# Kernel tuning notes

Hardware: AMD Instinct MI355X
Metric: run time of the kernel (lower is better)

## Reference

```python
import jax, jax.numpy as jnp
import numpy as np

NEG_SLOPE = 0.2  # PyG GATConv default negative_slope


def _gat_layer(x, src, dst, n_nodes, W, a_src, a_dst, b):
    # x: [N, din]; src/dst: [E] (self-loops already included)
    h = x @ W                                  # [N, dout]
    s_src = h @ a_src                          # [N]
    s_dst = h @ a_dst                          # [N]
    e = jax.nn.leaky_relu(s_src[src] + s_dst[dst], NEG_SLOPE)  # [E]
    # per-target-node softmax over incoming edges (stable via segment max)
    m = jax.ops.segment_max(e, dst, num_segments=n_nodes)      # [N]
    a = jnp.exp(e - m[dst])                    # [E]
    denom = jax.ops.segment_sum(a, dst, num_segments=n_nodes)  # [N]
    msg = h[src] * a[:, None]                  # [E, dout]
    agg = jax.ops.segment_sum(msg, dst, num_segments=n_nodes)  # [N, dout]
    return agg / denom[:, None] + b


def setup_inputs() -> dict:
    key = jax.random.key(0)
    ks = jax.random.split(key, 16)
    N, E = 100000, 1600000
    in_dim, hid_dim, out_dim = 128, 128, 64
    x = jax.random.normal(ks[0], (N, in_dim), dtype=jnp.float32)
    edge_idx = jax.random.randint(ks[1], (2, E), 0, N, dtype=jnp.int32)

    def lin(k, din, dout):
        return jax.random.normal(k, (din, dout), dtype=jnp.float32) * (1.0 / np.sqrt(din))

    def att(k, dout):
        return jax.random.normal(k, (dout,), dtype=jnp.float32) * (1.0 / np.sqrt(dout))

    return {
        "x": x, "edge_idx": edge_idx,
        "W1": lin(ks[2], in_dim, hid_dim), "as1": att(ks[3], hid_dim), "ad1": att(ks[4], hid_dim), "b1": jnp.zeros((hid_dim,), jnp.float32),
        "W2": lin(ks[5], hid_dim, hid_dim), "as2": att(ks[6], hid_dim), "ad2": att(ks[7], hid_dim), "b2": jnp.zeros((hid_dim,), jnp.float32),
        "W3": lin(ks[8], hid_dim, out_dim), "as3": att(ks[9], out_dim), "ad3": att(ks[10], out_dim), "b3": jnp.zeros((out_dim,), jnp.float32),
    }


def reference(x, edge_idx, W1, as1, ad1, b1, W2, as2, ad2, b2, W3, as3, ad3, b3):
    N = x.shape[0]
    # add self-loops (PyG GATConv default add_self_loops=True)
    loops = jnp.arange(N, dtype=edge_idx.dtype)
    src = jnp.concatenate([edge_idx[0], loops])
    dst = jnp.concatenate([edge_idx[1], loops])
    h = _gat_layer(x, src, dst, N, W1, as1, ad1, b1)
    h = _gat_layer(h, src, dst, N, W2, as2, ad2, b2)
    h = _gat_layer(h, src, dst, N, W3, as3, ad3, b3)
    return jnp.mean(h, axis=-2)  # [out_dim]
```

## Files before the change

kernel.cpp:

```cpp
#include <hip/hip_runtime.h>

static inline int ceil_div(long long a, long long b) { return (int)((a + b - 1) / b); }

typedef __attribute__((ext_vector_type(8))) short bf16x8;
typedef __attribute__((ext_vector_type(4))) float f32x4;

#define TILE 8192
#define BKSH 9

__device__ __forceinline__ float lrelu(float t) { return t > 0.f ? t : 0.2f * t; }

__device__ __forceinline__ void atomAddF(float* p, float v) {
  unsafeAtomicAdd(p, v);
}

__device__ __forceinline__ unsigned int f2bf(float f) {
  unsigned int u = __float_as_uint(f);
  unsigned int r = ((u >> 16) & 1u) + 0x7fffu;
  return (u + r) >> 16;
}

__global__ void cvt_bf16(const float* __restrict__ X, unsigned short* __restrict__ Xb, int n4) {
  int i = blockIdx.x * blockDim.x + threadIdx.x;
  if (i < n4) {
    const float4 v = ((const float4*)X)[i];
    uint2 o;
    o.x = f2bf(v.x) | (f2bf(v.y) << 16);
    o.y = f2bf(v.z) | (f2bf(v.w) << 16);
    ((uint2*)Xb)[i] = o;
  }
}

__global__ void transpose_w(const float* __restrict__ W, unsigned short* __restrict__ Wt,
                            int DINv, int DOUTv) {
  int idx = blockIdx.x * blockDim.x + threadIdx.x;
  if (idx < DINv * DOUTv) {
    int k = idx / DOUTv, n = idx % DOUTv;
    Wt[n * DINv + k] = (unsigned short)f2bf(W[idx]);
  }
}

template<int DOUT>
__launch_bounds__(256)
__global__ void gemm_mfma(const unsigned short* __restrict__ Xb, const unsigned short* __restrict__ Wt,
                          const float* __restrict__ avs, const float* __restrict__ avd,
                          unsigned short* __restrict__ Hb, float* __restrict__ Ss,
                          float* __restrict__ Sd, int N, int RG) {
  constexpr int DIN = 128;
  constexpr int CG = DOUT / 64;
  const int wave = (int)((blockIdx.x * (unsigned)blockDim.x + threadIdx.x) >> 6);
  const int rg = wave / CG;
  const int cg = wave % CG;
  if (rg >= RG) return;
  const int lane = threadIdx.x & 63;
  const int l16 = lane & 15, quad = lane >> 4;
  const int row0 = rg * 64, colw0 = cg * 64;

  int xoff[4], woff[4];
#pragma unroll
  for (int t = 0; t < 4; t++) {
    int m = row0 + t * 16 + l16; if (m > N - 1) m = N - 1;
    xoff[t] = m * DIN + quad * 8;
    woff[t] = (colw0 + t * 16 + l16) * DIN + quad * 8;
  }

  f32x4 acc[4][4];
#pragma unroll
  for (int a = 0; a < 4; a++)
#pragma unroll
    for (int c = 0; c < 4; c++) acc[a][c] = (f32x4)0.f;

#pragma unroll
  for (int kk = 0; kk < 4; kk++) {
    bf16x8 aw[4], bx[4];
#pragma unroll
    for (int t = 0; t < 4; t++) aw[t] = *(const bf16x8*)(Wt + woff[t] + kk * 32);
#pragma unroll
    for (int t = 0; t < 4; t++) bx[t] = *(const bf16x8*)(Xb + xoff[t] + kk * 32);
#pragma unroll
    for (int wt = 0; wt < 4; wt++)
#pragma unroll
      for (int xt = 0; xt < 4; xt++)
        acc[wt][xt] = __builtin_amdgcn_mfma_f32_16x16x32_bf16(aw[wt], bx[xt], acc[wt][xt], 0, 0, 0);
  }

  float4 af[4], df[4];
#pragma unroll
  for (int wt = 0; wt < 4; wt++) {
    af[wt] = *(const float4*)(avs + colw0 + wt * 16 + quad * 4);
    df[wt] = *(const float4*)(avd + colw0 + wt * 16 + quad * 4);
  }
#pragma unroll
  for (int xt = 0; xt < 4; xt++) {
    const int m = row0 + xt * 16 + l16;
    float ps = 0.f, pd = 0.f;
#pragma unroll
    for (int wt = 0; wt < 4; wt++) {
      const f32x4 c = acc[wt][xt];
      ps += c[0]*af[wt].x + c[1]*af[wt].y + c[2]*af[wt].z + c[3]*af[wt].w;
      pd += c[0]*df[wt].x + c[1]*df[wt].y + c[2]*df[wt].z + c[3]*df[wt].w;
    }
    ps += __shfl_xor(ps, 16); ps += __shfl_xor(ps, 32);
    pd += __shfl_xor(pd, 16); pd += __shfl_xor(pd, 32);
    if (quad == 0 && m < N) { atomAddF(&Ss[m], ps); atomAddF(&Sd[m], pd); }
    if (m < N) {
      unsigned short* hp = Hb + (size_t)m * DOUT + colw0 + quad * 4;
#pragma unroll
      for (int wt = 0; wt < 4; wt++) {
        const f32x4 c = acc[wt][xt];
        uint2 o;
        o.x = f2bf(c[0]) | (f2bf(c[1]) << 16);
        o.y = f2bf(c[2]) | (f2bf(c[3]) << 16);
        *(uint2*)(hp + wt * 16) = o;
      }
    }
  }
}

__launch_bounds__(256)
__global__ void bucket_hist(const int* __restrict__ dstv, int* __restrict__ bh,
                            int E, int NBUK) {
  __shared__ int h[256];
  h[threadIdx.x] = 0;
  __syncthreads();
  const int base = blockIdx.x * TILE;
  const int end = min(E, base + TILE);
  for (int i = base + threadIdx.x; i < end; i += 256)
    atomicAdd(&h[dstv[i] >> BKSH], 1);
  __syncthreads();
  if (threadIdx.x < NBUK) bh[blockIdx.x * NBUK + threadIdx.x] = h[threadIdx.x];
}

__launch_bounds__(256)
__global__ void col_scan(int* __restrict__ bh, int* __restrict__ tot, int NBA, int NBUK) {
  __shared__ int sc[256];
  const int t = threadIdx.x;
  const int b = blockIdx.x;
  int carry = 0;
  for (int c0 = 0; c0 < NBA; c0 += 256) {
    const int idx = c0 + t;
    const int v = (idx < NBA) ? bh[idx * NBUK + b] : 0;
    sc[t] = v;
    __syncthreads();
    for (int off = 1; off < 256; off <<= 1) {
      int u = (t >= off) ? sc[t - off] : 0;
      __syncthreads();
      sc[t] += u;
      __syncthreads();
    }
    if (idx < NBA) bh[idx * NBUK + b] = carry + sc[t] - v;
    carry += sc[255];
    __syncthreads();
  }
  if (t == 0) tot[b] = carry;
}

__launch_bounds__(256)
__global__ void base_scan(const int* __restrict__ tot, int* __restrict__ bucketBase,
                          int* __restrict__ rowptr_N, int NBUK, int E) {
  __shared__ int sc[256];
  const int t = threadIdx.x;
  int carry = 0;
  for (int c0 = 0; c0 < NBUK; c0 += 256) {
    const int idx = c0 + t;
    const int v = (idx < NBUK) ? tot[idx] : 0;
    sc[t] = v;
    __syncthreads();
    for (int off = 1; off < 256; off <<= 1) {
      int u = (t >= off) ? sc[t - off] : 0;
      __syncthreads();
      sc[t] += u;
      __syncthreads();
    }
    if (idx < NBUK) bucketBase[idx] = carry + sc[t] - v;
    carry += sc[255];
    __syncthreads();
  }
  if (t == 0) { bucketBase[NBUK] = E; *rowptr_N = E; }
}

__launch_bounds__(256)
__global__ void bucket_scatter(const int* __restrict__ src, const int* __restrict__ dstv,
                               const int* __restrict__ bh, const int* __restrict__ bucketBase,
                               unsigned int* __restrict__ pairs, int E, int NBUK) {
  __shared__ int ofs[256];
  if (threadIdx.x < NBUK)
    ofs[threadIdx.x] = bh[blockIdx.x * NBUK + threadIdx.x] + bucketBase[threadIdx.x];
  __syncthreads();
  const int base = blockIdx.x * TILE;
  const int end = min(E, base + TILE);
  for (int i = base + threadIdx.x; i < end; i += 256) {
    const int d = dstv[i];
    const int pos = atomicAdd(&ofs[d >> BKSH], 1);
    pairs[pos] = ((unsigned int)src[i] << BKSH) | (unsigned int)(d & ((1 << BKSH) - 1));
  }
}

__launch_bounds__(256)
__global__ void region_build(const unsigned int* __restrict__ pairs,
                             const int* __restrict__ bucketBase,
                             int* __restrict__ rowptr, int* __restrict__ srcs, int N) {
  __shared__ int cnt[512], ofs[512], ps[256];
  const int t = threadIdx.x;
  const int r = blockIdx.x;
  const int p0 = bucketBase[r], p1 = bucketBase[r + 1];
  cnt[t] = 0; cnt[t + 256] = 0;
  __syncthreads();
  for (int i = p0 + t; i < p1; i += 256)
    atomicAdd(&cnt[pairs[i] & 511u], 1);
  __syncthreads();
  const int c0 = cnt[2 * t], c1 = cnt[2 * t + 1];
  const int pr = c0 + c1;
  ps[t] = pr;
  __syncthreads();
  for (int off = 1; off < 256; off <<= 1) {
    int v = (t >= off) ? ps[t - off] : 0;
    __syncthreads();
    ps[t] += v;
    __syncthreads();
  }
  const int pbase = ps[t] - pr;
  ofs[2 * t] = pbase; ofs[2 * t + 1] = pbase + c0;
  __syncthreads();
  {
    const int d0 = (r << BKSH) + t;
    if (d0 < N) rowptr[d0] = p0 + ofs[t];
    const int d1 = (r << BKSH) + t + 256;
    if (d1 < N) rowptr[d1] = p0 + ofs[t + 256];
  }
  __syncthreads();
  for (int i = p0 + t; i < p1; i += 256) {
    const unsigned int w = pairs[i];
    const int pos = atomicAdd(&ofs[w & 511u], 1);
    srcs[p0 + pos] = (int)(w >> BKSH);
  }
}

template<int DOUT, bool OBF>
__launch_bounds__(256)
__global__ void node_gather(const int* __restrict__ rowptr, const int* __restrict__ srcs,
                            const float* __restrict__ Ss, const float* __restrict__ Sd,
                            const unsigned short* __restrict__ Hb, const float* __restrict__ b,
                            float* __restrict__ out, unsigned short* __restrict__ outb, int N) {
  constexpr int EPL = DOUT / 16;
  constexpr int CAP = 64;
  __shared__ uint2 swL[16][CAP];

  const int l16 = threadIdx.x & 15;
  const int grp = threadIdx.x >> 4;
  const int node = blockIdx.x * 16 + grp;
  if (node >= N) return;

  const int r0 = rowptr[node], r1 = rowptr[node + 1];
  const int deg = r1 - r0;
  const int degc = min(deg, CAP);
  const float sd = Sd[node];
  const float eself = lrelu(Ss[node] + sd);

  float m = eself;
  for (int j0 = 0; j0 < deg; j0 += 16) {
    const int idx = j0 + l16;
    float e = -1e30f;
    if (idx < deg) {
      const int s = srcs[r0 + idx];
      e = lrelu(Ss[s] + sd);
      if (idx < CAP) swL[grp][idx] = make_uint2((unsigned)s, __float_as_uint(e));
    }
    m = fmaxf(m, e);
  }
#pragma unroll
  for (int off = 8; off; off >>= 1) m = fmaxf(m, __shfl_xor(m, off));

  const float wself = __expf(eself - m);
  float lsum = 0.f;
  for (int j0 = 0; j0 < degc; j0 += 16) {
    const int idx = j0 + l16;
    if (idx < degc) {
      uint2 sw = swL[grp][idx];
      const float w = __expf(__uint_as_float(sw.y) - m);
      sw.y = __float_as_uint(w);
      swL[grp][idx] = sw;
      lsum += w;
    }
  }
  for (int j0 = CAP; j0 < deg; j0 += 16) {
    const int idx = j0 + l16;
    if (idx < deg) {
      const int s = srcs[r0 + idx];
      lsum += __expf(lrelu(Ss[s] + sd) - m);
    }
  }
#pragma unroll
  for (int off = 8; off; off >>= 1) lsum += __shfl_xor(lsum, off);
  const float inv = 1.f / (lsum + wself);
  __syncthreads();

  float acc[EPL];
#pragma unroll
  for (int k = 0; k < EPL; k++) acc[k] = 0.f;

  const size_t colb = (size_t)l16 * EPL;
  int j = 0;
  for (; j + 4 <= degc; j += 4) {
    uint2 sw0 = swL[grp][j], sw1 = swL[grp][j+1], sw2 = swL[grp][j+2], sw3 = swL[grp][j+3];
    const unsigned short* p0 = Hb + (size_t)sw0.x * DOUT + colb;
    const unsigned short* p1 = Hb + (size_t)sw1.x * DOUT + colb;
    const unsigned short* p2 = Hb + (size_t)sw2.x * DOUT + colb;
    const unsigned short* p3 = Hb + (size_t)sw3.x * DOUT + colb;
    if (EPL == 8) {
      const uint4 u0 = *(const uint4*)p0, u1 = *(const uint4*)p1;
      const uint4 u2 = *(const uint4*)p2, u3 = *(const uint4*)p3;
      const float w0 = __uint_as_float(sw0.y), w1 = __uint_as_float(sw1.y);
      const float w2 = __uint_as_float(sw2.y), w3 = __uint_as_float(sw3.y);
      const unsigned int a0[4] = {u0.x,u0.y,u0.z,u0.w}, a1[4] = {u1.x,u1.y,u1.z,u1.w};
      const unsigned int a2[4] = {u2.x,u2.y,u2.z,u2.w}, a3[4] = {u3.x,u3.y,u3.z,u3.w};
#pragma unroll
      for (int k = 0; k < 4; k++) {
        acc[2*k]   += __uint_as_float(a0[k] << 16) * w0 + __uint_as_float(a1[k] << 16) * w1
                    + __uint_as_float(a2[k] << 16) * w2 + __uint_as_float(a3[k] << 16) * w3;
        acc[2*k+1] += __uint_as_float(a0[k] & 0xffff0000u) * w0 + __uint_as_float(a1[k] & 0xffff0000u) * w1
                    + __uint_as_float(a2[k] & 0xffff0000u) * w2 + __uint_as_float(a3[k] & 0xffff0000u) * w3;
      }
    } else {
      const uint2 u0 = *(const uint2*)p0, u1 = *(const uint2*)p1;
      const uint2 u2 = *(const uint2*)p2, u3 = *(const uint2*)p3;
      const float w0 = __uint_as_float(sw0.y), w1 = __uint_as_float(sw1.y);
      const float w2 = __uint_as_float(sw2.y), w3 = __uint_as_float(sw3.y);
      const unsigned int a0[2] = {u0.x,u0.y}, a1[2] = {u1.x,u1.y};
      const unsigned int a2[2] = {u2.x,u2.y}, a3[2] = {u3.x,u3.y};
#pragma unroll
      for (int k = 0; k < 2; k++) {
        acc[2*k]   += __uint_as_float(a0[k] << 16) * w0 + __uint_as_float(a1[k] << 16) * w1
                    + __uint_as_float(a2[k] << 16) * w2 + __uint_as_float(a3[k] << 16) * w3;
        acc[2*k+1] += __uint_as_float(a0[k] & 0xffff0000u) * w0 + __uint_as_float(a1[k] & 0xffff0000u) * w1
                    + __uint_as_float(a2[k] & 0xffff0000u) * w2 + __uint_as_float(a3[k] & 0xffff0000u) * w3;
      }
    }
  }
  for (; j < degc; j++) {
    const uint2 sw = swL[grp][j];
    const float w = __uint_as_float(sw.y);
    const unsigned short* pp = Hb + (size_t)sw.x * DOUT + colb;
#pragma unroll
    for (int k = 0; k < EPL / 2; k++) {
      const unsigned int u = ((const unsigned int*)pp)[k];
      acc[2*k]   += __uint_as_float(u << 16) * w;
      acc[2*k+1] += __uint_as_float(u & 0xffff0000u) * w;
    }
  }
  for (j = CAP; j < deg; j++) {
    const int s = srcs[r0 + j];
    const float w = __expf(lrelu(Ss[s] + sd) - m);
    const unsigned short* pp = Hb + (size_t)s * DOUT + colb;
#pragma unroll
    for (int k = 0; k < EPL / 2; k++) {
      const unsigned int u = ((const unsigned int*)pp)[k];
      acc[2*k]   += __uint_as_float(u << 16) * w;
      acc[2*k+1] += __uint_as_float(u & 0xffff0000u) * w;
    }
  }
  {
    const unsigned short* pp = Hb + (size_t)node * DOUT + colb;
#pragma unroll
    for (int k = 0; k < EPL / 2; k++) {
      const unsigned int u = ((const unsigned int*)pp)[k];
      acc[2*k]   += __uint_as_float(u << 16) * wself;
      acc[2*k+1] += __uint_as_float(u & 0xffff0000u) * wself;
    }
  }

  float o[EPL];
#pragma unroll
  for (int k = 0; k < EPL; k++) o[k] = acc[k] * inv + b[colb + k];
  if (OBF) {
    if (EPL == 8) {
      uint4 u;
      u.x = f2bf(o[0]) | (f2bf(o[1]) << 16);
      u.y = f2bf(o[2]) | (f2bf(o[3]) << 16);
      u.z = f2bf(o[4]) | (f2bf(o[5]) << 16);
      u.w = f2bf(o[6]) | (f2bf(o[7]) << 16);
      *(uint4*)(outb + (size_t)node * DOUT + colb) = u;
    } else {
      uint2 u;
      u.x = f2bf(o[0]) | (f2bf(o[1]) << 16);
      u.y = f2bf(o[2]) | (f2bf(o[3]) << 16);
      *(uint2*)(outb + (size_t)node * DOUT + colb) = u;
    }
  } else {
    float* op = out + (size_t)node * DOUT + colb;
#pragma unroll
    for (int k = 0; k < EPL; k += 4)
      *(float4*)(op + k) = make_float4(o[k], o[k+1], o[k+2], o[k+3]);
  }
}

__global__ void mean64(const float* __restrict__ Hf, float* __restrict__ out, int N, float scale) {
  __shared__ float sm[256];
  const int col = threadIdx.x & 63;
  const int seg = threadIdx.x >> 6;
  const int stride = gridDim.x * 4;
  float s = 0.f;
  for (int n = blockIdx.x * 4 + seg; n < N; n += stride) s += Hf[(size_t)n * 64 + col];
  sm[threadIdx.x] = s;
  __syncthreads();
  if (seg == 0) {
    float tot = sm[col] + sm[64 + col] + sm[128 + col] + sm[192 + col];
    atomAddF(&out[col], tot * scale);
  }
}

extern "C" void kernel_launch(void* const* d_in, const int* in_sizes, int n_in,
                              void* d_out, int out_size, void* d_ws, size_t ws_size,
                              hipStream_t stream) {
  const float* x   = (const float*)d_in[0];
  const int*   ei  = (const int*)d_in[1];
  const float* W1  = (const float*)d_in[2];
  const float* as1 = (const float*)d_in[3];
  const float* ad1 = (const float*)d_in[4];
  const float* b1  = (const float*)d_in[5];
  const float* W2  = (const float*)d_in[6];
  const float* as2 = (const float*)d_in[7];
  const float* ad2 = (const float*)d_in[8];
  const float* b2  = (const float*)d_in[9];
  const float* W3  = (const float*)d_in[10];
  const float* as3 = (const float*)d_in[11];
  const float* ad3 = (const float*)d_in[12];
  const float* b3  = (const float*)d_in[13];

  const int N = in_sizes[0] / 128;
  const int E = in_sizes[1] / 2;
  const int* src  = ei;
  const int* dstv = ei + E;
  const int RG = ceil_div(N, 64);
  const int NBA = ceil_div(E, TILE);
  const int NBUK = ceil_div(N, 1 << BKSH);

  float* p = (float*)d_ws;
  float* bufA = p; p += (size_t)N * 64;
  float* SsSd = p; p += (size_t)2 * N;
  float* Ss = SsSd, *Sd = SsSd + N;
  unsigned short* Xb = (unsigned short*)p; p += (size_t)N * 64;
  unsigned short* Hb = (unsigned short*)p; p += (size_t)N * 64;
  unsigned short* Wt1 = (unsigned short*)p; p += 128 * 128 / 2;
  unsigned short* Wt2 = (unsigned short*)p; p += 128 * 128 / 2;
  unsigned short* Wt3 = (unsigned short*)p; p += 128 * 64 / 2;
  int* ip = (int*)p;
  int* rowptr     = ip; ip += N + 1;
  int* bh         = ip; ip += (size_t)NBA * NBUK;
  int* tot        = ip; ip += NBUK;
  int* bucketBase = ip; ip += NBUK + 1;
  unsigned int* pairs = (unsigned int*)ip; ip += E;
  int* srcs       = ip; ip += E;

  bucket_hist<<<NBA, 256, 0, stream>>>(dstv, bh, E, NBUK);
  col_scan<<<NBUK, 256, 0, stream>>>(bh, tot, NBA, NBUK);
  base_scan<<<1, 256, 0, stream>>>(tot, bucketBase, rowptr + N, NBUK, E);
  bucket_scatter<<<NBA, 256, 0, stream>>>(src, dstv, bh, bucketBase, pairs, E, NBUK);
  region_build<<<NBUK, 256, 0, stream>>>(pairs, bucketBase, rowptr, srcs, N);

  transpose_w<<<ceil_div(128 * 128, 256), 256, 0, stream>>>(W1, Wt1, 128, 128);
  transpose_w<<<ceil_div(128 * 128, 256), 256, 0, stream>>>(W2, Wt2, 128, 128);
  transpose_w<<<ceil_div(128 * 64, 256), 256, 0, stream>>>(W3, Wt3, 128, 64);
  cvt_bf16<<<ceil_div((long long)N * 32, 256), 256, 0, stream>>>(x, Xb, N * 32);

  const int GG = ceil_div(N, 16);
  hipMemsetAsync(SsSd, 0, (size_t)2 * N * sizeof(float), stream);
  gemm_mfma<128><<<ceil_div((long long)RG * 2, 4), 256, 0, stream>>>(Xb, Wt1, as1, ad1, Hb, Ss, Sd, N, RG);
  node_gather<128, true><<<GG, 256, 0, stream>>>(rowptr, srcs, Ss, Sd, Hb, b1, nullptr, Xb, N);
  hipMemsetAsync(SsSd, 0, (size_t)2 * N * sizeof(float), stream);
  gemm_mfma<128><<<ceil_div((long long)RG * 2, 4), 256, 0, stream>>>(Xb, Wt2, as2, ad2, Hb, Ss, Sd, N, RG);
  node_gather<128, true><<<GG, 256, 0, stream>>>(rowptr, srcs, Ss, Sd, Hb, b2, nullptr, Xb, N);
  hipMemsetAsync(SsSd, 0, (size_t)2 * N * sizeof(float), stream);
  gemm_mfma<64><<<ceil_div((long long)RG, 4), 256, 0, stream>>>(Xb, Wt3, as3, ad3, Hb, Ss, Sd, N, RG);
  node_gather<64, false><<<GG, 256, 0, stream>>>(rowptr, srcs, Ss, Sd, Hb, b3, bufA, nullptr, N);

  hipMemsetAsync(d_out, 0, 64 * sizeof(float), stream);
  mean64<<<256, 256, 0, stream>>>(bufA, (float*)d_out, N, 1.0f / (float)N);
}
```

Baseline: 449.2 us.

## Compute full GEMM rows per wave, drop score atomics and memsets, widen gather unroll

Each wave in the GEMM now computes all output columns for its 64 rows. The attention scores can then be reduced fully in registers and written with plain stores, which removes the float atomics and the three memsets that zeroed Ss/Sd. The three weight-transpose launches are merged into one kernel. The node gather loop now issues 8 independent neighbour row loads per iteration instead of 4 to raise memory-level parallelism, and the shared edge buffer is padded. The GEMM uses more accumulator registers per wave and launches half as many waves, which may reduce occupancy and parallelism.

```diff
diff --git a/kernel.cpp b/kernel.cpp
--- a/kernel.cpp
+++ b/kernel.cpp
@@ -31,87 +31,91 @@
   }
 }
 
-__global__ void transpose_w(const float* __restrict__ W, unsigned short* __restrict__ Wt,
-                            int DINv, int DOUTv) {
+__global__ void transpose_all(const float* __restrict__ W1, const float* __restrict__ W2,
+                              const float* __restrict__ W3, unsigned short* __restrict__ Wt1,
+                              unsigned short* __restrict__ Wt2, unsigned short* __restrict__ Wt3) {
   int idx = blockIdx.x * blockDim.x + threadIdx.x;
-  if (idx < DINv * DOUTv) {
-    int k = idx / DOUTv, n = idx % DOUTv;
-    Wt[n * DINv + k] = (unsigned short)f2bf(W[idx]);
-  }
+  const float* W; unsigned short* Wt; int local, DOUTv;
+  if (idx < 16384)      { W = W1; Wt = Wt1; local = idx;          DOUTv = 128; }
+  else if (idx < 32768) { W = W2; Wt = Wt2; local = idx - 16384;  DOUTv = 128; }
+  else if (idx < 40960) { W = W3; Wt = Wt3; local = idx - 32768;  DOUTv = 64;  }
+  else return;
+  const int k = local / DOUTv, n = local % DOUTv;
+  Wt[n * 128 + k] = (unsigned short)f2bf(W[local]);
 }
 
 template<int DOUT>
-__launch_bounds__(256)
-__global__ void gemm_mfma(const unsigned short* __restrict__ Xb, const unsigned short* __restrict__ Wt,
+__launch_bounds__(256, 2)
+__global__ void gemm_full(const unsigned short* __restrict__ Xb, const unsigned short* __restrict__ Wt,
                           const float* __restrict__ avs, const float* __restrict__ avd,
                           unsigned short* __restrict__ Hb, float* __restrict__ Ss,
                           float* __restrict__ Sd, int N, int RG) {
   constexpr int DIN = 128;
-  constexpr int CG = DOUT / 64;
-  const int wave = (int)((blockIdx.x * (unsigned)blockDim.x + threadIdx.x) >> 6);
-  const int rg = wave / CG;
-  const int cg = wave % CG;
+  constexpr int NWT = DOUT / 16;
+  const int rg = (int)((blockIdx.x * (unsigned)blockDim.x + threadIdx.x) >> 6);
   if (rg >= RG) return;
   const int lane = threadIdx.x & 63;
   const int l16 = lane & 15, quad = lane >> 4;
-  const int row0 = rg * 64, colw0 = cg * 64;
-
-  int xoff[4], woff[4];
+  const int row0 = rg * 64;
+
+  int xoff[4], woff[NWT];
 #pragma unroll
   for (int t = 0; t < 4; t++) {
     int m = row0 + t * 16 + l16; if (m > N - 1) m = N - 1;
     xoff[t] = m * DIN + quad * 8;
-    woff[t] = (colw0 + t * 16 + l16) * DIN + quad * 8;
-  }
-
-  f32x4 acc[4][4];
-#pragma unroll
-  for (int a = 0; a < 4; a++)
-#pragma unroll
-    for (int c = 0; c < 4; c++) acc[a][c] = (f32x4)0.f;
+  }
+#pragma unroll
+  for (int w = 0; w < NWT; w++) woff[w] = (w * 16 + l16) * DIN + quad * 8;
+
+  f32x4 acc[NWT][4];
+#pragma unroll
+  for (int w = 0; w < NWT; w++)
+#pragma unroll
+    for (int c = 0; c < 4; c++) acc[w][c] = (f32x4)0.f;
 
 #pragma unroll
   for (int kk = 0; kk < 4; kk++) {
-    bf16x8 aw[4], bx[4];
-#pragma unroll
-    for (int t = 0; t < 4; t++) aw[t] = *(const bf16x8*)(Wt + woff[t] + kk * 32);
+    bf16x8 bx[4], aw[NWT];
 #pragma unroll
     for (int t = 0; t < 4; t++) bx[t] = *(const bf16x8*)(Xb + xoff[t] + kk * 32);
 #pragma unroll
-    for (int wt = 0; wt < 4; wt++)
+    for (int w = 0; w < NWT; w++) aw[w] = *(const bf16x8*)(Wt + woff[w] + kk * 32);
+#pragma unroll
+    for (int w = 0; w < NWT; w++)
 #pragma unroll
       for (int xt = 0; xt < 4; xt++)
-        acc[wt][xt] = __builtin_amdgcn_mfma_f32_16x16x32_bf16(aw[wt], bx[xt], acc[wt][xt], 0, 0, 0);
-  }
-
-  float4 af[4], df[4];
-#pragma unroll
-  for (int wt = 0; wt < 4; wt++) {
-    af[wt] = *(const float4*)(avs + colw0 + wt * 16 + quad * 4);
-    df[wt] = *(const float4*)(avd + colw0 + wt * 16 + quad * 4);
+        acc[w][xt] = __builtin_amdgcn_mfma_f32_16x16x32_bf16(aw[w], bx[xt], acc[w][xt], 0, 0, 0);
+  }
+
+  float ps[4] = {0.f, 0.f, 0.f, 0.f}, pd[4] = {0.f, 0.f, 0.f, 0.f};
+#pragma unroll
+  for (int w = 0; w < NWT; w++) {
+    const float4 af = *(const float4*)(avs + w * 16 + quad * 4);
+    const float4 df = *(const float4*)(avd + w * 16 + quad * 4);
+#pragma unroll
+    for (int xt = 0; xt < 4; xt++) {
+      const f32x4 c = acc[w][xt];
+      ps[xt] += c[0]*af.x + c[1]*af.y + c[2]*af.z + c[3]*af.w;
+      pd[xt] += c[0]*df.x + c[1]*df.y + c[2]*df.z + c[3]*df.w;
+    }
   }
 #pragma unroll
   for (int xt = 0; xt < 4; xt++) {
     const int m = row0 + xt * 16 + l16;
-    float ps = 0.f, pd = 0.f;
-#pragma unroll
-    for (int wt = 0; wt < 4; wt++) {
-      const f32x4 c = acc[wt][xt];
-      ps += c[0]*af[wt].x + c[1]*af[wt].y + c[2]*af[wt].z + c[3]*af[wt].w;
-      pd += c[0]*df[wt].x + c[1]*df[wt].y + c[2]*df[wt].z + c[3]*df[wt].w;
-    }
-    ps += __shfl_xor(ps, 16); ps += __shfl_xor(ps, 32);
-    pd += __shfl_xor(pd, 16); pd += __shfl_xor(pd, 32);
-    if (quad == 0 && m < N) { atomAddF(&Ss[m], ps); atomAddF(&Sd[m], pd); }
+    float p1 = ps[xt] + __shfl_xor(ps[xt], 16);
+    p1 += __shfl_xor(p1, 32);
+    float p2 = pd[xt] + __shfl_xor(pd[xt], 16);
+    p2 += __shfl_xor(p2, 32);
+    if (quad == 0 && m < N) { Ss[m] = p1; Sd[m] = p2; }
     if (m < N) {
-      unsigned short* hp = Hb + (size_t)m * DOUT + colw0 + quad * 4;
-#pragma unroll
-      for (int wt = 0; wt < 4; wt++) {
-        const f32x4 c = acc[wt][xt];
+      unsigned short* hp = Hb + (size_t)m * DOUT + quad * 4;
+#pragma unroll
+      for (int w = 0; w < NWT; w++) {
+        const f32x4 c = acc[w][xt];
         uint2 o;
         o.x = f2bf(c[0]) | (f2bf(c[1]) << 16);
         o.y = f2bf(c[2]) | (f2bf(c[3]) << 16);
-        *(uint2*)(hp + wt * 16) = o;
+        *(uint2*)(hp + w * 16) = o;
       }
     }
   }
@@ -244,7 +248,7 @@
                             float* __restrict__ out, unsigned short* __restrict__ outb, int N) {
   constexpr int EPL = DOUT / 16;
   constexpr int CAP = 64;
-  __shared__ uint2 swL[16][CAP];
+  __shared__ uint2 swL[16][CAP + 2];
 
   const int l16 = threadIdx.x & 15;
   const int grp = threadIdx.x >> 4;
@@ -301,39 +305,55 @@
 
   const size_t colb = (size_t)l16 * EPL;
   int j = 0;
-  for (; j + 4 <= degc; j += 4) {
-    uint2 sw0 = swL[grp][j], sw1 = swL[grp][j+1], sw2 = swL[grp][j+2], sw3 = swL[grp][j+3];
-    const unsigned short* p0 = Hb + (size_t)sw0.x * DOUT + colb;
-    const unsigned short* p1 = Hb + (size_t)sw1.x * DOUT + colb;
-    const unsigned short* p2 = Hb + (size_t)sw2.x * DOUT + colb;
-    const unsigned short* p3 = Hb + (size_t)sw3.x * DOUT + colb;
+  for (; j + 8 <= degc; j += 8) {
+    uint2 sw[8];
+#pragma unroll
+    for (int g = 0; g < 8; g++) sw[g] = swL[grp][j + g];
     if (EPL == 8) {
-      const uint4 u0 = *(const uint4*)p0, u1 = *(const uint4*)p1;
-      const uint4 u2 = *(const uint4*)p2, u3 = *(const uint4*)p3;
-      const float w0 = __uint_as_float(sw0.y), w1 = __uint_as_float(sw1.y);
-      const float w2 = __uint_as_float(sw2.y), w3 = __uint_as_float(sw3.y);
-      const unsigned int a0[4] = {u0.x,u0.y,u0.z,u0.w}, a1[4] = {u1.x,u1.y,u1.z,u1.w};
-      const unsigned int a2[4] = {u2.x,u2.y,u2.z,u2.w}, a3[4] = {u3.x,u3.y,u3.z,u3.w};
-#pragma unroll
-      for (int k = 0; k < 4; k++) {
-        acc[2*k]   += __uint_as_float(a0[k] << 16) * w0 + __uint_as_float(a1[k] << 16) * w1
-                    + __uint_as_float(a2[k] << 16) * w2 + __uint_as_float(a3[k] << 16) * w3;
-        acc[2*k+1] += __uint_as_float(a0[k] & 0xffff0000u) * w0 + __uint_as_float(a1[k] & 0xffff0000u) * w1
-                    + __uint_as_float(a2[k] & 0xffff0000u) * w2 + __uint_as_float(a3[k] & 0xffff0000u) * w3;
+      uint4 uu[8];
+#pragma unroll
+      for (int g = 0; g < 8; g++)
+        uu[g] = *(const uint4*)(Hb + (size_t)sw[g].x * DOUT + colb);
+#pragma unroll
+      for (int g = 0; g < 8; g++) {
+        const float w = __uint_as_float(sw[g].y);
+        const unsigned int a[4] = {uu[g].x, uu[g].y, uu[g].z, uu[g].w};
+#pragma unroll
+        for (int k = 0; k < 4; k++) {
+          acc[2*k]   += __uint_as_float(a[k] << 16) * w;
+          acc[2*k+1] += __uint_as_float(a[k] & 0xffff0000u) * w;
+        }
       }
     } else {
-      const uint2 u0 = *(const uint2*)p0, u1 = *(const uint2*)p1;
-      const uint2 u2 = *(const uint2*)p2, u3 = *(const uint2*)p3;
-      const float w0 = __uint_as_float(sw0.y), w1 = __uint_as_float(sw1.y);
-      const float w2 = __uint_as_float(sw2.y), w3 = __uint_as_float(sw3.y);
-      const unsigned int a0[2] = {u0.x,u0.y}, a1[2] = {u1.x,u1.y};
-      const unsigned int a2[2] = {u2.x,u2.y}, a3[2] = {u3.x,u3.y};
-#pragma unroll
-      for (int k = 0; k < 2; k++) {
-        acc[2*k]   += __uint_as_float(a0[k] << 16) * w0 + __uint_as_float(a1[k] << 16) * w1
-                    + __uint_as_float(a2[k] << 16) * w2 + __uint_as_float(a3[k] << 16) * w3;
-        acc[2*k+1] += __uint_as_float(a0[k] & 0xffff0000u) * w0 + __uint_as_float(a1[k] & 0xffff0000u) * w1
-                    + __uint_as_float(a2[k] & 0xffff0000u) * w2 + __uint_as_float(a3[k] & 0xffff0000u) * w3;
+      uint2 uu[8];
+#pragma unroll
+      for (int g = 0; g < 8; g++)
+        uu[g] = *(const uint2*)(Hb + (size_t)sw[g].x * DOUT + colb);
+#pragma unroll
+      for (int g = 0; g < 8; g++) {
+        const float w = __uint_as_float(sw[g].y);
+        const unsigned int a[2] = {uu[g].x, uu[g].y};
+#pragma unroll
+        for (int k = 0; k < 2; k++) {
+          acc[2*k]   += __uint_as_float(a[k] << 16) * w;
+          acc[2*k+1] += __uint_as_float(a[k] & 0xffff0000u) * w;
+        }
+      }
+    }
+  }
+  for (; j + 4 <= degc; j += 4) {
+    uint2 sw[4];
+#pragma unroll
+    for (int g = 0; g < 4; g++) sw[g] = swL[grp][j + g];
+#pragma unroll
+    for (int g = 0; g < 4; g++) {
+      const float w = __uint_as_float(sw[g].y);
+      const unsigned short* pp = Hb + (size_t)sw[g].x * DOUT + colb;
+#pragma unroll
+      for (int k = 0; k < EPL / 2; k++) {
+        const unsigned int u = ((const unsigned int*)pp)[k];
+        acc[2*k]   += __uint_as_float(u << 16) * w;
+        acc[2*k+1] += __uint_as_float(u & 0xffff0000u) * w;
       }
     }
   }
@@ -458,20 +478,16 @@
   bucket_scatter<<<NBA, 256, 0, stream>>>(src, dstv, bh, bucketBase, pairs, E, NBUK);
   region_build<<<NBUK, 256, 0, stream>>>(pairs, bucketBase, rowptr, srcs, N);
 
-  transpose_w<<<ceil_div(128 * 128, 256), 256, 0, stream>>>(W1, Wt1, 128, 128);
-  transpose_w<<<ceil_div(128 * 128, 256), 256, 0, stream>>>(W2, Wt2, 128, 128);
-  transpose_w<<<ceil_div(128 * 64, 256), 256, 0, stream>>>(W3, Wt3, 128, 64);
+  transpose_all<<<ceil_div(40960, 256), 256, 0, stream>>>(W1, W2, W3, Wt1, Wt2, Wt3);
   cvt_bf16<<<ceil_div((long long)N * 32, 256), 256, 0, stream>>>(x, Xb, N * 32);
 
   const int GG = ceil_div(N, 16);
-  hipMemsetAsync(SsSd, 0, (size_t)2 * N * sizeof(float), stream);
-  gemm_mfma<128><<<ceil_div((long long)RG * 2, 4), 256, 0, stream>>>(Xb, Wt1, as1, ad1, Hb, Ss, Sd, N, RG);
+  const int GB = ceil_div(RG, 4);
+  gemm_full<128><<<GB, 256, 0, stream>>>(Xb, Wt1, as1, ad1, Hb, Ss, Sd, N, RG);
   node_gather<128, true><<<GG, 256, 0, stream>>>(rowptr, srcs, Ss, Sd, Hb, b1, nullptr, Xb, N);
-  hipMemsetAsync(SsSd, 0, (size_t)2 * N * sizeof(float), stream);
-  gemm_mfma<128><<<ceil_div((long long)RG * 2, 4), 256, 0, stream>>>(Xb, Wt2, as2, ad2, Hb, Ss, Sd, N, RG);
+  gemm_full<128><<<GB, 256, 0, stream>>>(Xb, Wt2, as2, ad2, Hb, Ss, Sd, N, RG);
   node_gather<128, true><<<GG, 256, 0, stream>>>(rowptr, srcs, Ss, Sd, Hb, b2, nullptr, Xb, N);
-  hipMemsetAsync(SsSd, 0, (size_t)2 * N * sizeof(float), stream);
-  gemm_mfma<64><<<ceil_div((long long)RG, 4), 256, 0, stream>>>(Xb, Wt3, as3, ad3, Hb, Ss, Sd, N, RG);
+  gemm_full<64><<<GB, 256, 0, stream>>>(Xb, Wt3, as3, ad3, Hb, Ss, Sd, N, RG);
   node_gather<64, false><<<GG, 256, 0, stream>>>(rowptr, srcs, Ss, Sd, Hb, b3, bufA, nullptr, N);
 
   hipMemsetAsync(d_out, 0, 64 * sizeof(float), stream);
```

Measured after the change: 453.0 us. No clear change (+0.9%).

## Single-pass attention gather without max subtraction, atomic-free score reduction

Applied to the files above, without the earlier changes.

The node gather drops the segment-max pass and the 64-entry shared cache. Each 16-edge chunk now computes exp(lrelu) weights, stages them in shared memory and accumulates the features in one pass, instead of separate max, exp-sum and accumulate passes. The GEMM combines the two column halves of the attention scores through shared memory instead of atomics, so the per-layer memsets go away, and the three weight-transpose launches are merged into one. Skipping the max subtraction gives up the numerical-stability guard and could overflow exp for large attention logits.

```diff
diff --git a/kernel.cpp b/kernel.cpp
--- a/kernel.cpp
+++ b/kernel.cpp
@@ -31,13 +31,17 @@
   }
 }
 
-__global__ void transpose_w(const float* __restrict__ W, unsigned short* __restrict__ Wt,
-                            int DINv, int DOUTv) {
+__global__ void transpose_all(const float* __restrict__ W1, const float* __restrict__ W2,
+                              const float* __restrict__ W3, unsigned short* __restrict__ Wt1,
+                              unsigned short* __restrict__ Wt2, unsigned short* __restrict__ Wt3) {
   int idx = blockIdx.x * blockDim.x + threadIdx.x;
-  if (idx < DINv * DOUTv) {
-    int k = idx / DOUTv, n = idx % DOUTv;
-    Wt[n * DINv + k] = (unsigned short)f2bf(W[idx]);
-  }
+  const float* W; unsigned short* Wt; int local, DOUTv;
+  if (idx < 16384)      { W = W1; Wt = Wt1; local = idx;          DOUTv = 128; }
+  else if (idx < 32768) { W = W2; Wt = Wt2; local = idx - 16384;  DOUTv = 128; }
+  else if (idx < 40960) { W = W3; Wt = Wt3; local = idx - 32768;  DOUTv = 64;  }
+  else return;
+  const int k = local / DOUTv, n = local % DOUTv;
+  Wt[n * 128 + k] = (unsigned short)f2bf(W[local]);
 }
 
 template<int DOUT>
@@ -48,70 +52,93 @@
                           float* __restrict__ Sd, int N, int RG) {
   constexpr int DIN = 128;
   constexpr int CG = DOUT / 64;
-  const int wave = (int)((blockIdx.x * (unsigned)blockDim.x + threadIdx.x) >> 6);
-  const int rg = wave / CG;
-  const int cg = wave % CG;
-  if (rg >= RG) return;
+  constexpr int RPB = 4 / CG;
+  __shared__ float sps[RPB][2][64], spd[RPB][2][64];
+
+  const int wv = threadIdx.x >> 6;
+  const int rgl = wv / CG;
+  const int cg  = wv % CG;
+  const int rg = blockIdx.x * RPB + rgl;
+  const bool active = rg < RG;
   const int lane = threadIdx.x & 63;
   const int l16 = lane & 15, quad = lane >> 4;
   const int row0 = rg * 64, colw0 = cg * 64;
 
-  int xoff[4], woff[4];
-#pragma unroll
-  for (int t = 0; t < 4; t++) {
-    int m = row0 + t * 16 + l16; if (m > N - 1) m = N - 1;
-    xoff[t] = m * DIN + quad * 8;
-    woff[t] = (colw0 + t * 16 + l16) * DIN + quad * 8;
-  }
-
-  f32x4 acc[4][4];
-#pragma unroll
-  for (int a = 0; a < 4; a++)
-#pragma unroll
-    for (int c = 0; c < 4; c++) acc[a][c] = (f32x4)0.f;
-
-#pragma unroll
-  for (int kk = 0; kk < 4; kk++) {
-    bf16x8 aw[4], bx[4];
-#pragma unroll
-    for (int t = 0; t < 4; t++) aw[t] = *(const bf16x8*)(Wt + woff[t] + kk * 32);
-#pragma unroll
-    for (int t = 0; t < 4; t++) bx[t] = *(const bf16x8*)(Xb + xoff[t] + kk * 32);
-#pragma unroll
-    for (int wt = 0; wt < 4; wt++)
-#pragma unroll
-      for (int xt = 0; xt < 4; xt++)
-        acc[wt][xt] = __builtin_amdgcn_mfma_f32_16x16x32_bf16(aw[wt], bx[xt], acc[wt][xt], 0, 0, 0);
-  }
-
-  float4 af[4], df[4];
-#pragma unroll
-  for (int wt = 0; wt < 4; wt++) {
-    af[wt] = *(const float4*)(avs + colw0 + wt * 16 + quad * 4);
-    df[wt] = *(const float4*)(avd + colw0 + wt * 16 + quad * 4);
-  }
-#pragma unroll
-  for (int xt = 0; xt < 4; xt++) {
-    const int m = row0 + xt * 16 + l16;
-    float ps = 0.f, pd = 0.f;
+  if (active) {
+    int xoff[4], woff[4];
+#pragma unroll
+    for (int t = 0; t < 4; t++) {
+      int m = row0 + t * 16 + l16; if (m > N - 1) m = N - 1;
+      xoff[t] = m * DIN + quad * 8;
+      woff[t] = (colw0 + t * 16 + l16) * DIN + quad * 8;
+    }
+
+    f32x4 acc[4][4];
+#pragma unroll
+    for (int a = 0; a < 4; a++)
+#pragma unroll
+      for (int c = 0; c < 4; c++) acc[a][c] = (f32x4)0.f;
+
+#pragma unroll
+    for (int kk = 0; kk < 4; kk++) {
+      bf16x8 aw[4], bx[4];
+#pragma unroll
+      for (int t = 0; t < 4; t++) aw[t] = *(const bf16x8*)(Wt + woff[t] + kk * 32);
+#pragma unroll
+      for (int t = 0; t < 4; t++) bx[t] = *(const bf16x8*)(Xb + xoff[t] + kk * 32);
+#pragma unroll
+      for (int wt = 0; wt < 4; wt++)
+#pragma unroll
+        for (int xt = 0; xt < 4; xt++)
+          acc[wt][xt] = __builtin_amdgcn_mfma_f32_16x16x32_bf16(aw[wt], bx[xt], acc[wt][xt], 0, 0, 0);
+    }
+
+    float4 af[4], df[4];
 #pragma unroll
     for (int wt = 0; wt < 4; wt++) {
-      const f32x4 c = acc[wt][xt];
-      ps += c[0]*af[wt].x + c[1]*af[wt].y + c[2]*af[wt].z + c[3]*af[wt].w;
-      pd += c[0]*df[wt].x + c[1]*df[wt].y + c[2]*df[wt].z + c[3]*df[wt].w;
-    }
-    ps += __shfl_xor(ps, 16); ps += __shfl_xor(ps, 32);
-    pd += __shfl_xor(pd, 16); pd += __shfl_xor(pd, 32);
-    if (quad == 0 && m < N) { atomAddF(&Ss[m], ps); atomAddF(&Sd[m], pd); }
-    if (m < N) {
-      unsigned short* hp = Hb + (size_t)m * DOUT + colw0 + quad * 4;
+      af[wt] = *(const float4*)(avs + colw0 + wt * 16 + quad * 4);
+      df[wt] = *(const float4*)(avd + colw0 + wt * 16 + quad * 4);
+    }
+#pragma unroll
+    for (int xt = 0; xt < 4; xt++) {
+      const int m = row0 + xt * 16 + l16;
+      float ps = 0.f, pd = 0.f;
 #pragma unroll
       for (int wt = 0; wt < 4; wt++) {
         const f32x4 c = acc[wt][xt];
-        uint2 o;
-        o.x = f2bf(c[0]) | (f2bf(c[1]) << 16);
-        o.y = f2bf(c[2]) | (f2bf(c[3]) << 16);
-        *(uint2*)(hp + wt * 16) = o;
+        ps += c[0]*af[wt].x + c[1]*af[wt].y + c[2]*af[wt].z + c[3]*af[wt].w;
+        pd += c[0]*df[wt].x + c[1]*df[wt].y + c[2]*df[wt].z + c[3]*df[wt].w;
+      }
+      ps += __shfl_xor(ps, 16); ps += __shfl_xor(ps, 32);
+      pd += __shfl_xor(pd, 16); pd += __shfl_xor(pd, 32);
+      if (quad == 0) {
+        if (CG == 2) {
+          sps[rgl][cg][xt * 16 + l16] = ps;
+          spd[rgl][cg][xt * 16 + l16] = pd;
+        } else if (m < N) {
+          Ss[m] = ps; Sd[m] = pd;
+        }
+      }
+      if (m < N) {
+        unsigned short* hp = Hb + (size_t)m * DOUT + colw0 + quad * 4;
+#pragma unroll
+        for (int wt = 0; wt < 4; wt++) {
+          const f32x4 c = acc[wt][xt];
+          uint2 o;
+          o.x = f2bf(c[0]) | (f2bf(c[1]) << 16);
+          o.y = f2bf(c[2]) | (f2bf(c[3]) << 16);
+          *(uint2*)(hp + wt * 16) = o;
+        }
+      }
+    }
+  }
+  if (CG == 2) {
+    __syncthreads();
+    if (active && cg == 0) {
+      const int m = row0 + lane;
+      if (m < N) {
+        Ss[m] = sps[rgl][0][lane] + sps[rgl][1][lane];
+        Sd[m] = spd[rgl][0][lane] + spd[rgl][1][lane];
       }
     }
   }
@@ -243,8 +270,7 @@
                             const unsigned short* __restrict__ Hb, const float* __restrict__ b,
                             float* __restrict__ out, unsigned short* __restrict__ outb, int N) {
   constexpr int EPL = DOUT / 16;
-  constexpr int CAP = 64;
-  __shared__ uint2 swL[16][CAP];
+  __shared__ uint2 swL[16][18];
 
   const int l16 = threadIdx.x & 15;
   const int grp = threadIdx.x >> 4;
@@ -253,112 +279,77 @@
 
   const int r0 = rowptr[node], r1 = rowptr[node + 1];
   const int deg = r1 - r0;
-  const int degc = min(deg, CAP);
   const float sd = Sd[node];
-  const float eself = lrelu(Ss[node] + sd);
-
-  float m = eself;
+  const float wself = __expf(lrelu(Ss[node] + sd));
+
+  float acc[EPL];
+#pragma unroll
+  for (int k = 0; k < EPL; k++) acc[k] = 0.f;
+  float lsum = 0.f;
+  const size_t colb = (size_t)l16 * EPL;
+
   for (int j0 = 0; j0 < deg; j0 += 16) {
     const int idx = j0 + l16;
-    float e = -1e30f;
+    int s = node; float w = 0.f;
     if (idx < deg) {
-      const int s = srcs[r0 + idx];
-      e = lrelu(Ss[s] + sd);
-      if (idx < CAP) swL[grp][idx] = make_uint2((unsigned)s, __float_as_uint(e));
-    }
-    m = fmaxf(m, e);
-  }
-#pragma unroll
-  for (int off = 8; off; off >>= 1) m = fmaxf(m, __shfl_xor(m, off));
-
-  const float wself = __expf(eself - m);
-  float lsum = 0.f;
-  for (int j0 = 0; j0 < degc; j0 += 16) {
-    const int idx = j0 + l16;
-    if (idx < degc) {
-      uint2 sw = swL[grp][idx];
-      const float w = __expf(__uint_as_float(sw.y) - m);
-      sw.y = __float_as_uint(w);
-      swL[grp][idx] = sw;
-      lsum += w;
-    }
-  }
-  for (int j0 = CAP; j0 < deg; j0 += 16) {
-    const int idx = j0 + l16;
-    if (idx < deg) {
-      const int s = srcs[r0 + idx];
-      lsum += __expf(lrelu(Ss[s] + sd) - m);
-    }
-  }
-#pragma unroll
-  for (int off = 8; off; off >>= 1) lsum += __shfl_xor(lsum, off);
-  const float inv = 1.f / (lsum + wself);
-  __syncthreads();
-
-  float acc[EPL];
-#pragma unroll
-  for (int k = 0; k < EPL; k++) acc[k] = 0.f;
-
-  const size_t colb = (size_t)l16 * EPL;
-  int j = 0;
-  for (; j + 4 <= degc; j += 4) {
-    uint2 sw0 = swL[grp][j], sw1 = swL[grp][j+1], sw2 = swL[grp][j+2], sw3 = swL[grp][j+3];
-    const unsigned short* p0 = Hb + (size_t)sw0.x * DOUT + colb;
-    const unsigned short* p1 = Hb + (size_t)sw1.x * DOUT + colb;
-    const unsigned short* p2 = Hb + (size_t)sw2.x * DOUT + colb;
-    const unsigned short* p3 = Hb + (size_t)sw3.x * DOUT + colb;
-    if (EPL == 8) {
-      const uint4 u0 = *(const uint4*)p0, u1 = *(const uint4*)p1;
-      const uint4 u2 = *(const uint4*)p2, u3 = *(const uint4*)p3;
+      s = srcs[r0 + idx];
+      w = __expf(lrelu(Ss[s] + sd));
+    }
+    lsum += w;
+    swL[grp][l16] = make_uint2((unsigned)s, __float_as_uint(w));
+    const int cnt = min(16, deg - j0);
+    int t = 0;
+    for (; t + 4 <= cnt; t += 4) {
+      const uint2 sw0 = swL[grp][t],     sw1 = swL[grp][t + 1];
+      const uint2 sw2 = swL[grp][t + 2], sw3 = swL[grp][t + 3];
       const float w0 = __uint_as_float(sw0.y), w1 = __uint_as_float(sw1.y);
       const float w2 = __uint_as_float(sw2.y), w3 = __uint_as_float(sw3.y);
-      const unsigned int a0[4] = {u0.x,u0.y,u0.z,u0.w}, a1[4] = {u1.x,u1.y,u1.z,u1.w};
-      const unsigned int a2[4] = {u2.x,u2.y,u2.z,u2.w}, a3[4] = {u3.x,u3.y,u3.z,u3.w};
-#pragma unroll
-      for (int k = 0; k < 4; k++) {
-        acc[2*k]   += __uint_as_float(a0[k] << 16) * w0 + __uint_as_float(a1[k] << 16) * w1
-                    + __uint_as_float(a2[k] << 16) * w2 + __uint_as_float(a3[k] << 16) * w3;
-        acc[2*k+1] += __uint_as_float(a0[k] & 0xffff0000u) * w0 + __uint_as_float(a1[k] & 0xffff0000u) * w1
-                    + __uint_as_float(a2[k] & 0xffff0000u) * w2 + __uint_as_float(a3[k] & 0xffff0000u) * w3;
-      }
-    } else {
-      const uint2 u0 = *(const uint2*)p0, u1 = *(const uint2*)p1;
-      const uint2 u2 = *(const uint2*)p2, u3 = *(const uint2*)p3;
-      const float w0 = __uint_as_float(sw0.y), w1 = __uint_as_float(sw1.y);
-      const float w2 = __uint_as_float(sw2.y), w3 = __uint_as_float(sw3.y);
-      const unsigned int a0[2] = {u0.x,u0.y}, a1[2] = {u1.x,u1.y};
-      const unsigned int a2[2] = {u2.x,u2.y}, a3[2] = {u3.x,u3.y};
-#pragma unroll
-      for (int k = 0; k < 2; k++) {
-        acc[2*k]   += __uint_as_float(a0[k] << 16) * w0 + __uint_as_float(a1[k] << 16) * w1
-                    + __uint_as_float(a2[k] << 16) * w2 + __uint_as_float(a3[k] << 16) * w3;
-        acc[2*k+1] += __uint_as_float(a0[k] & 0xffff0000u) * w0 + __uint_as_float(a1[k] & 0xffff0000u) * w1
-                    + __uint_as_float(a2[k] & 0xffff0000u) * w2 + __uint_as_float(a3[k] & 0xffff0000u) * w3;
-      }
-    }
-  }
-  for (; j < degc; j++) {
-    const uint2 sw = swL[grp][j];
-    const float w = __uint_as_float(sw.y);
-    const unsigned short* pp = Hb + (size_t)sw.x * DOUT + colb;
-#pragma unroll
-    for (int k = 0; k < EPL / 2; k++) {
-      const unsigned int u = ((const unsigned int*)pp)[k];
-      acc[2*k]   += __uint_as_float(u << 16) * w;
-      acc[2*k+1] += __uint_as_float(u & 0xffff0000u) * w;
-    }
-  }
-  for (j = CAP; j < deg; j++) {
-    const int s = srcs[r0 + j];
-    const float w = __expf(lrelu(Ss[s] + sd) - m);
-    const unsigned short* pp = Hb + (size_t)s * DOUT + colb;
-#pragma unroll
-    for (int k = 0; k < EPL / 2; k++) {
-      const unsigned int u = ((const unsigned int*)pp)[k];
-      acc[2*k]   += __uint_as_float(u << 16) * w;
-      acc[2*k+1] += __uint_as_float(u & 0xffff0000u) * w;
-    }
-  }
+      if (EPL == 8) {
+        const uint4 u0 = *(const uint4*)(Hb + (size_t)sw0.x * DOUT + colb);
+        const uint4 u1 = *(const uint4*)(Hb + (size_t)sw1.x * DOUT + colb);
+        const uint4 u2 = *(const uint4*)(Hb + (size_t)sw2.x * DOUT + colb);
+        const uint4 u3 = *(const uint4*)(Hb + (size_t)sw3.x * DOUT + colb);
+        const unsigned int a0[4] = {u0.x,u0.y,u0.z,u0.w}, a1[4] = {u1.x,u1.y,u1.z,u1.w};
+        const unsigned int a2[4] = {u2.x,u2.y,u2.z,u2.w}, a3[4] = {u3.x,u3.y,u3.z,u3.w};
+#pragma unroll
+        for (int k = 0; k < 4; k++) {
+          acc[2*k]   += __uint_as_float(a0[k] << 16) * w0 + __uint_as_float(a1[k] << 16) * w1
+                      + __uint_as_float(a2[k] << 16) * w2 + __uint_as_float(a3[k] << 16) * w3;
+          acc[2*k+1] += __uint_as_float(a0[k] & 0xffff0000u) * w0 + __uint_as_float(a1[k] & 0xffff0000u) * w1
+                      + __uint_as_float(a2[k] & 0xffff0000u) * w2 + __uint_as_float(a3[k] & 0xffff0000u) * w3;
+        }
+      } else {
+        const uint2 u0 = *(const uint2*)(Hb + (size_t)sw0.x * DOUT + colb);
+        const uint2 u1 = *(const uint2*)(Hb + (size_t)sw1.x * DOUT + colb);
+        const uint2 u2 = *(const uint2*)(Hb + (size_t)sw2.x * DOUT + colb);
+        const uint2 u3 = *(const uint2*)(Hb + (size_t)sw3.x * DOUT + colb);
+        const unsigned int a0[2] = {u0.x,u0.y}, a1[2] = {u1.x,u1.y};
+        const unsigned int a2[2] = {u2.x,u2.y}, a3[2] = {u3.x,u3.y};
+#pragma unroll
+        for (int k = 0; k < 2; k++) {
+          acc[2*k]   += __uint_as_float(a0[k] << 16) * w0 + __uint_as_float(a1[k] << 16) * w1
+                      + __uint_as_float(a2[k] << 16) * w2 + __uint_as_float(a3[k] << 16) * w3;
+          acc[2*k+1] += __uint_as_float(a0[k] & 0xffff0000u) * w0 + __uint_as_float(a1[k] & 0xffff0000u) * w1
+                      + __uint_as_float(a2[k] & 0xffff0000u) * w2 + __uint_as_float(a3[k] & 0xffff0000u) * w3;
+        }
+      }
+    }
+    for (; t < cnt; t++) {
+      const uint2 sw = swL[grp][t];
+      const float w0 = __uint_as_float(sw.y);
+      const unsigned short* pp = Hb + (size_t)sw.x * DOUT + colb;
+#pragma unroll
+      for (int k = 0; k < EPL / 2; k++) {
+        const unsigned int u = ((const unsigned int*)pp)[k];
+        acc[2*k]   += __uint_as_float(u << 16) * w0;
+        acc[2*k+1] += __uint_as_float(u & 0xffff0000u) * w0;
+      }
+    }
+  }
+
+#pragma unroll
+  for (int off = 8; off; off >>= 1) lsum += __shfl_xor(lsum, off);
+
   {
     const unsigned short* pp = Hb + (size_t)node * DOUT + colb;
 #pragma unroll
@@ -368,6 +359,7 @@
       acc[2*k+1] += __uint_as_float(u & 0xffff0000u) * wself;
     }
   }
+  const float inv = 1.f / (lsum + wself);
 
   float o[EPL];
 #pragma unroll
@@ -458,20 +450,15 @@
   bucket_scatter<<<NBA, 256, 0, stream>>>(src, dstv, bh, bucketBase, pairs, E, NBUK);
   region_build<<<NBUK, 256, 0, stream>>>(pairs, bucketBase, rowptr, srcs, N);
 
-  transpose_w<<<ceil_div(128 * 128, 256), 256, 0, stream>>>(W1, Wt1, 128, 128);
-  transpose_w<<<ceil_div(128 * 128, 256), 256, 0, stream>>>(W2, Wt2, 128, 128);
-  transpose_w<<<ceil_div(128 * 64, 256), 256, 0, stream>>>(W3, Wt3, 128, 64);
+  transpose_all<<<ceil_div(40960, 256), 256, 0, stream>>>(W1, W2, W3, Wt1, Wt2, Wt3);
   cvt_bf16<<<ceil_div((long long)N * 32, 256), 256, 0, stream>>>(x, Xb, N * 32);
 
   const int GG = ceil_div(N, 16);
-  hipMemsetAsync(SsSd, 0, (size_t)2 * N * sizeof(float), stream);
-  gemm_mfma<128><<<ceil_div((long long)RG * 2, 4), 256, 0, stream>>>(Xb, Wt1, as1, ad1, Hb, Ss, Sd, N, RG);
+  gemm_mfma<128><<<ceil_div(RG, 2), 256, 0, stream>>>(Xb, Wt1, as1, ad1, Hb, Ss, Sd, N, RG);
   node_gather<128, true><<<GG, 256, 0, stream>>>(rowptr, srcs, Ss, Sd, Hb, b1, nullptr, Xb, N);
-  hipMemsetAsync(SsSd, 0, (size_t)2 * N * sizeof(float), stream);
-  gemm_mfma<128><<<ceil_div((long long)RG * 2, 4), 256, 0, stream>>>(Xb, Wt2, as2, ad2, Hb, Ss, Sd, N, RG);
+  gemm_mfma<128><<<ceil_div(RG, 2), 256, 0, stream>>>(Xb, Wt2, as2, ad2, Hb, Ss, Sd, N, RG);
   node_gather<128, true><<<GG, 256, 0, stream>>>(rowptr, srcs, Ss, Sd, Hb, b2, nullptr, Xb, N);
-  hipMemsetAsync(SsSd, 0, (size_t)2 * N * sizeof(float), stream);
-  gemm_mfma<64><<<ceil_div((long long)RG, 4), 256, 0, stream>>>(Xb, Wt3, as3, ad3, Hb, Ss, Sd, N, RG);
+  gemm_mfma<64><<<ceil_div(RG, 4), 256, 0, stream>>>(Xb, Wt3, as3, ad3, Hb, Ss, Sd, N, RG);
   node_gather<64, false><<<GG, 256, 0, stream>>>(rowptr, srcs, Ss, Sd, Hb, b3, bufA, nullptr, N);
 
   hipMemsetAsync(d_out, 0, 64 * sizeof(float), stream);
```

New measurement: 437.7 us. 1.03x faster.
